# Kernel optimization log

Hardware: AMD Instinct MI355X
Metric: run time of the kernel (lower is better)

Reference implementation:

```python
import jax, jax.numpy as jnp
import numpy as np

B, T, C, H, N = 2, 1024, 1024, 16, 64
D_DECAY, D_AAA, D_MV, D_GATE = 64, 64, 32, 128
LN_EPS = 64e-5  # GroupNorm eps used by RWKV7 (1e-5 * head_size_divisor**2)


def setup_inputs():
    key = jax.random.key(0)
    ks = jax.random.split(key, 32)
    rn = lambda k, shape, s=1.0: jax.random.normal(k, shape, jnp.float32) * s
    p = {}
    p['x'] = rn(ks[0], (B, T, C))
    p['v_first'] = rn(ks[1], (B, T, C))
    for i, nm in enumerate(['x_r', 'x_w', 'x_k', 'x_v', 'x_a', 'x_g']):
        p[nm] = jax.random.uniform(ks[2 + i], (1, 1, C), jnp.float32)
    p['w1'] = rn(ks[8], (C, D_DECAY), 0.02); p['w2'] = rn(ks[9], (D_DECAY, C), 0.02); p['w0'] = rn(ks[10], (C,), 0.5)
    p['a1'] = rn(ks[11], (C, D_AAA), 0.02); p['a2'] = rn(ks[12], (D_AAA, C), 0.02); p['a0'] = rn(ks[13], (C,), 0.1)
    p['v1'] = rn(ks[14], (C, D_MV), 0.02); p['v2'] = rn(ks[15], (D_MV, C), 0.02); p['v0'] = rn(ks[16], (C,), 0.1)
    p['g1'] = rn(ks[17], (C, D_GATE), 0.02); p['g2'] = rn(ks[18], (D_GATE, C), 0.02)
    p['k_k'] = jax.random.uniform(ks[19], (1, 1, C), jnp.float32)
    p['k_a'] = jax.random.uniform(ks[20], (1, 1, C), jnp.float32)
    p['r_k'] = rn(ks[21], (H, N), 0.1)
    s = C ** -0.5
    p['W_r'] = rn(ks[22], (C, C), s); p['W_k'] = rn(ks[23], (C, C), s)
    p['W_v'] = rn(ks[24], (C, C), s); p['W_o'] = rn(ks[25], (C, C), s)
    p['ln_w'] = jnp.ones((C,), jnp.float32); p['ln_b'] = jnp.zeros((C,), jnp.float32)
    return p


def _rwkv7_op(r, w, k, v, a, b):
    # r,w,k,v,a,b: (B,T,C). Per-head matrix-state recurrence:
    #   S_t = S_{t-1} * diag(decay_t) + (S_{t-1} @ a_t) b_t^T + v_t k_t^T ; out_t = S_t @ r_t
    f = lambda z: z.reshape(B, T, H, N).astype(jnp.float32).transpose(1, 0, 2, 3)  # (T,B,H,N)
    r_, k_, v_, a_, b_ = f(r), f(k), f(v), f(a), f(b)
    d_ = jnp.exp(-jnp.exp(f(w)))  # decay in (0,1)

    def step(S, inp):
        rt, dt, kt, vt, at, bt = inp  # each (B,H,N)
        sa = jnp.einsum('bhij,bhj->bhi', S, at)
        S = S * dt[:, :, None, :] + sa[..., None] * bt[:, :, None, :] + vt[..., None] * kt[:, :, None, :]
        return S, jnp.einsum('bhij,bhj->bhi', S, rt)

    S0 = jnp.zeros((B, H, N, N), jnp.float32)
    _, out = jax.lax.scan(step, S0, (r_, d_, k_, v_, a_, b_))
    return out.transpose(1, 0, 2, 3).reshape(B, T, C)


def _forward(x, v_first, x_r, x_w, x_k, x_v, x_a, x_g, w1, w2, w0, a1, a2, a0,
             v1, v2, v0, g1, g2, k_k, k_a, r_k, W_r, W_k, W_v, W_o, ln_w, ln_b):
    xx = jnp.pad(x, ((0, 0), (1, 0), (0, 0)))[:, :T] - x  # token shift
    xr = x + xx * x_r; xw = x + xx * x_w; xk = x + xx * x_k
    xv = x + xx * x_v; xa = x + xx * x_a; xg = x + xx * x_g
    r = xr @ W_r
    w = -jax.nn.softplus(-(jnp.tanh(xw @ w1) @ w2 + w0)) - 0.5
    k = xk @ W_k
    v = xv @ W_v
    v = v + (v_first - v) * jax.nn.sigmoid(xv @ v1 @ v2 + v0)  # layer_id > 0 branch
    a = jax.nn.sigmoid(xa @ a1 @ a2 + a0)
    g = jax.nn.sigmoid(xg @ g1) @ g2
    kk = (k * k_k).reshape(B, T, H, N)
    kk = (kk / jnp.maximum(jnp.linalg.norm(kk, axis=-1, keepdims=True), 1e-12)).reshape(B, T, C)
    k = k * (1.0 + (a - 1.0) * k_a)
    y = _rwkv7_op(r, w, k, v, -kk, kk * a)
    # GroupNorm(H groups over C) applied per token
    yh = y.reshape(B, T, H, N)
    mu = yh.mean(-1, keepdims=True)
    var = yh.var(-1, keepdims=True)
    y = ((yh - mu) / jnp.sqrt(var + LN_EPS)).reshape(B, T, C) * ln_w + ln_b
    rh = r.reshape(B, T, H, N); kh = k.reshape(B, T, H, N); vh = v.reshape(B, T, H, N)
    y = y + ((rh * kh * r_k).sum(-1, keepdims=True) * vh).reshape(B, T, C)
    return (y * g) @ W_o


def reference(x, v_first, x_r, x_w, x_k, x_v, x_a, x_g, w1, w2, w0, a1, a2, a0,
              v1, v2, v0, g1, g2, k_k, k_a, r_k, W_r, W_k, W_v, W_o, ln_w, ln_b):
    out = _forward(x, v_first, x_r, x_w, x_k, x_v, x_a, x_g, w1, w2, w0, a1, a2, a0,
                   v1, v2, v0, g1, g2, k_k, k_a, r_k, W_r, W_k, W_v, W_o, ln_w, ln_b)
    return (out, v_first)
```

## Files before the change

### kernel.cpp

```cpp
#include <hip/hip_runtime.h>
#include <hip/hip_bf16.h>
#include <cstdint>
#include <cstddef>

typedef __hip_bfloat16 bf16;
typedef __bf16 bf16x8 __attribute__((ext_vector_type(8)));
typedef float f32x4 __attribute__((ext_vector_type(4)));

#define BB 2
#define TT 1024
#define CC 1024
#define HH 16
#define PKS 448

__device__ __forceinline__ bf16 f2b(float v){ return __float2bfloat16(v); }

__device__ __forceinline__ float oct_add(float x) {
    x += __int_as_float(__builtin_amdgcn_mov_dpp(__float_as_int(x), 0xB1, 0xF, 0xF, true));
    x += __int_as_float(__builtin_amdgcn_mov_dpp(__float_as_int(x), 0x4E, 0xF, 0xF, true));
    x += __int_as_float(__builtin_amdgcn_mov_dpp(__float_as_int(x), 0x141, 0xF, 0xF, true));
    return x;
}

struct TrDesc { const float* in; bf16* out; int R, S; };
struct TrArgs { TrDesc d[12]; };

__global__ __launch_bounds__(256) void transpose_batch(TrArgs args)
{
    TrDesc t = args.d[blockIdx.z];
    __shared__ float tile[32][33];
    int s0 = blockIdx.x * 32, r0 = blockIdx.y * 32;
    if (s0 >= t.S || r0 >= t.R) return;
    int tx = threadIdx.x & 31, ty = threadIdx.x >> 5;
#pragma unroll
    for (int i = 0; i < 4; i++) {
        int r = r0 + ty + i * 8, s = s0 + tx;
        if (r < t.R && s < t.S) tile[ty + i * 8][tx] = t.in[(size_t)r * t.S + s];
    }
    __syncthreads();
#pragma unroll
    for (int i = 0; i < 4; i++) {
        int s = s0 + ty + i * 8, r = r0 + tx;
        if (s < t.S && r < t.R) t.out[(size_t)s * t.R + r] = f2b(tile[tx][ty + i * 8]);
    }
}

__global__ __launch_bounds__(256) void mix_kernel(
    const float* __restrict__ x, const float* __restrict__ vfirst,
    const float* __restrict__ mr, const float* __restrict__ mw, const float* __restrict__ mk,
    const float* __restrict__ mv, const float* __restrict__ ma, const float* __restrict__ mg,
    bf16* __restrict__ xr, bf16* __restrict__ xw, bf16* __restrict__ xk,
    bf16* __restrict__ xv, bf16* __restrict__ xa, bf16* __restrict__ xg,
    float* __restrict__ vout)
{
    int row = blockIdx.x;
    int t = row & (TT - 1);
    size_t base = (size_t)row * CC;
    for (int c = threadIdx.x; c < CC; c += 256) {
        float xc = x[base + c];
        float xp = (t > 0) ? x[base - CC + c] : 0.f;
        float d = xp - xc;
        xr[base + c] = f2b(xc + d * mr[c]);
        xw[base + c] = f2b(xc + d * mw[c]);
        xk[base + c] = f2b(xc + d * mk[c]);
        xv[base + c] = f2b(xc + d * mv[c]);
        xa[base + c] = f2b(xc + d * ma[c]);
        xg[base + c] = f2b(xc + d * mg[c]);
        vout[base + c] = vfirst[base + c];
    }
}

template <class EmitF>
__device__ __forceinline__ void gemm_tile(const bf16* __restrict__ A, const bf16* __restrict__ BT,
                                          int K, int m0, int n0, EmitF emit)
{
    __shared__ __align__(16) bf16 Atile[128 * 32];
    __shared__ __align__(16) bf16 Btile[128 * 32];
    int tid = threadIdx.x;
    int w = tid >> 6, lane = tid & 63;
    int wr = w >> 1, wc = w & 1;
    int quad = lane >> 4, l16 = lane & 15;

    f32x4 zero = {0.f, 0.f, 0.f, 0.f};
    f32x4 acc[4][4];
#pragma unroll
    for (int i = 0; i < 4; i++)
#pragma unroll
        for (int j = 0; j < 4; j++) acc[i][j] = zero;

    int rr = lane >> 2;
    int cs = lane & 3;
    int ra0 = w * 32 + rr;
    int ra1 = ra0 + 16;
    int cg0 = cs ^ ((ra0 >> 1) & 3);
    int cg1 = cs ^ ((ra1 >> 1) & 3);

    for (int k0 = 0; k0 < K; k0 += 32) {
        uint4 av0 = *reinterpret_cast<const uint4*>(A  + (size_t)(m0 + ra0) * K + k0 + cg0 * 8);
        uint4 av1 = *reinterpret_cast<const uint4*>(A  + (size_t)(m0 + ra1) * K + k0 + cg1 * 8);
        uint4 bv0 = *reinterpret_cast<const uint4*>(BT + (size_t)(n0 + ra0) * K + k0 + cg0 * 8);
        uint4 bv1 = *reinterpret_cast<const uint4*>(BT + (size_t)(n0 + ra1) * K + k0 + cg1 * 8);
        __syncthreads();
        *reinterpret_cast<uint4*>(&Atile[ra0 * 32 + cs * 8]) = av0;
        *reinterpret_cast<uint4*>(&Atile[ra1 * 32 + cs * 8]) = av1;
        *reinterpret_cast<uint4*>(&Btile[ra0 * 32 + cs * 8]) = bv0;
        *reinterpret_cast<uint4*>(&Btile[ra1 * 32 + cs * 8]) = bv1;
        __syncthreads();

        bf16x8 af[4], bfr[4];
#pragma unroll
        for (int mi = 0; mi < 4; mi++) {
            int m = wr * 64 + mi * 16 + l16;
            int c2 = quad ^ ((m >> 1) & 3);
            af[mi] = *reinterpret_cast<const bf16x8*>(&Atile[m * 32 + c2 * 8]);
        }
#pragma unroll
        for (int ni = 0; ni < 4; ni++) {
            int n = wc * 64 + ni * 16 + l16;
            int c2 = quad ^ ((n >> 1) & 3);
            bfr[ni] = *reinterpret_cast<const bf16x8*>(&Btile[n * 32 + c2 * 8]);
        }
#pragma unroll
        for (int mi = 0; mi < 4; mi++)
#pragma unroll
            for (int ni = 0; ni < 4; ni++)
                acc[mi][ni] = __builtin_amdgcn_mfma_f32_16x16x32_bf16(af[mi], bfr[ni], acc[mi][ni], 0, 0, 0);
    }

#pragma unroll
    for (int mi = 0; mi < 4; mi++)
#pragma unroll
        for (int ni = 0; ni < 4; ni++)
#pragma unroll
            for (int rg = 0; rg < 4; rg++) {
                int m = m0 + wr * 64 + mi * 16 + quad * 4 + rg;
                int n = n0 + wc * 64 + ni * 16 + l16;
                emit(m, n, acc[mi][ni][rg]);
            }
}

struct B3Args { const bf16* A[3]; const bf16* BT[3]; float* out[3]; };
__global__ __launch_bounds__(256) void big3_kernel(B3Args args)
{
    int z = blockIdx.z;
    float* out = args.out[z];
    gemm_tile(args.A[z], args.BT[z], 1024, blockIdx.x * 128, blockIdx.y * 128,
              [&](int m, int n, float v) { out[(size_t)m * 1024 + n] = v; });
}

struct L1Desc { const bf16* A; const bf16* BT; bf16* outB; int N; int mode; };
struct L1Args { L1Desc d[4]; };
__global__ __launch_bounds__(256) void lora1_kernel(L1Args args)
{
    L1Desc dz = args.d[blockIdx.z];
    gemm_tile(dz.A, dz.BT, 1024, blockIdx.x * 128, 0,
              [&](int m, int n, float v) {
                  if (n < dz.N) {
                      float r = (dz.mode == 2) ? tanhf(v)
                              : (dz.mode == 3) ? 1.f / (1.f + expf(-v)) : v;
                      dz.outB[(size_t)m * dz.N + n] = f2b(r);
                  }
              });
}

struct L2Desc { const bf16* A; const bf16* BT; const float* bias; float* outF; int K; int mode; };
struct L2Args { L2Desc d[4]; const float* vraw; const float* vfirst; };
__global__ __launch_bounds__(256) void lora2_kernel(L2Args args)
{
    L2Desc dz = args.d[blockIdx.z];
    gemm_tile(dz.A, dz.BT, dz.K, blockIdx.x * 128, blockIdx.y * 128,
              [&](int m, int n, float v) {
                  size_t idx = (size_t)m * 1024 + n;
                  if (dz.mode == 4) {
                      float xx = v + dz.bias[n];
                      float ww = -log1pf(expf(-xx)) - 0.5f;
                      dz.outF[idx] = expf(-expf(ww));
                  } else if (dz.mode == 5) {
                      float xx = v + dz.bias[n];
                      dz.outF[idx] = 1.f / (1.f + expf(-xx));
                  } else if (dz.mode == 6) {
                      float gate = 1.f / (1.f + expf(-(v + dz.bias[n])));
                      float vr = args.vraw[idx];
                      dz.outF[idx] = vr + (args.vfirst[idx] - vr) * gate;
                  } else {
                      dz.outF[idx] = v;
                  }
              });
}

__global__ __launch_bounds__(256) void final_kernel(const bf16* __restrict__ A, const bf16* __restrict__ BT,
                                                    float* __restrict__ out)
{
    gemm_tile(A, BT, 1024, blockIdx.x * 128, blockIdx.y * 128,
              [&](int m, int n, float v) { out[(size_t)m * 1024 + n] = v; });
}

__global__ __launch_bounds__(256) void pack_kernel(
    float* __restrict__ k, const float* __restrict__ a, const float* __restrict__ r,
    const float* __restrict__ v, const float* __restrict__ dw,
    const float* __restrict__ kkw, const float* __restrict__ kaw,
    float* __restrict__ PK)
{
    int tid = threadIdx.x;
    int wave = tid >> 6, lane = tid & 63;
    int idx = blockIdx.x * 4 + wave;
    size_t off = (size_t)idx * 64 + lane;
    int c = (idx & 15) * 64 + lane;
    float kraw = k[off];
    float av = a[off];
    float kkv = kraw * kkw[c];
    float s = kkv * kkv;
#pragma unroll
    for (int m = 32; m; m >>= 1) s += __shfl_xor(s, m);
    float kkn = kkv / fmaxf(sqrtf(s), 1e-12f);
    float ks = kraw * (1.f + (av - 1.f) * kaw[c]);
    k[off] = ks;
    float bb = kkn * av;
    float rv = r[off];
    float dv = dw[off];
    float bt = bb * rv, ct = ks * rv;
#pragma unroll
    for (int m = 32; m; m >>= 1) { bt += __shfl_xor(bt, m); ct += __shfl_xor(ct, m); }
    int b = idx >> 14;
    int h = idx & 15;
    int t = (idx >> 4) & (TT - 1);
    size_t sidx = (size_t)(b * HH + h) * TT + t;
    float* pw = PK + sidx * PKS;
    pw[lane] = ks; pw[64 + lane] = kkn; pw[128 + lane] = bb; pw[192 + lane] = v[off];
    pw[256 + lane] = rv; pw[320 + lane] = dv;
    if (lane == 0) { pw[384] = bt; pw[385] = ct; }
}

struct StepS {
    f32x4 q[2], d[2], r[2], k[2], b[2];
    float vi; float2 bc;
};

__device__ __forceinline__ void load_stepS(StepS& s, const float* __restrict__ sb, int jc, int row)
{
#pragma unroll
    for (int m = 0; m < 2; m++) s.q[m] = *(const f32x4*)(sb + 64 + jc + 4 * m);
#pragma unroll
    for (int m = 0; m < 2; m++) s.d[m] = *(const f32x4*)(sb + 320 + jc + 4 * m);
#pragma unroll
    for (int m = 0; m < 2; m++) s.r[m] = *(const f32x4*)(sb + 256 + jc + 4 * m);
#pragma unroll
    for (int m = 0; m < 2; m++) s.k[m] = *(const f32x4*)(sb + jc + 4 * m);
#pragma unroll
    for (int m = 0; m < 2; m++) s.b[m] = *(const f32x4*)(sb + 128 + jc + 4 * m);
    s.vi = sb[192 + row];
    s.bc = *(const float2*)(sb + 384);
}

__device__ __forceinline__ float step_updateS(const StepS& sd, f32x4 S[2])
{
    f32x4 Sd0 = S[0] * sd.d[0];
    f32x4 Sd1 = S[1] * sd.d[1];
    f32x4 sac = S[0] * sd.q[0] + S[1] * sd.q[1];
    f32x4 oac = Sd0 * sd.r[0] + Sd1 * sd.r[1];
    float sar = (sac[0] + sac[1]) + (sac[2] + sac[3]);
    sar = oct_add(sar);
    float od = oct_add((oac[0] + oac[1]) + (oac[2] + oac[3]));
    float o = fmaf(sd.vi, sd.bc.y, fmaf(-sar, sd.bc.x, od));
    float sa = -sar;
    S[0] = Sd0 + sa * sd.b[0] + sd.vi * sd.k[0];
    S[1] = Sd1 + sa * sd.b[1] + sd.vi * sd.k[1];
    return o;
}

__global__ __launch_bounds__(64, 1) void scan_kernel(
    const float* __restrict__ PK, float* __restrict__ ybuf)
{
    const int lane = threadIdx.x;
    const int bh = blockIdx.x >> 3;
    const int b = bh >> 4, h = bh & 15;
    const int wq = blockIdx.x & 7;
    const int row = wq * 8 + (lane >> 3);
    const int jc = (lane & 7) * 8;

    f32x4 S[2];
    S[0] = (f32x4){0.f, 0.f, 0.f, 0.f};
    S[1] = (f32x4){0.f, 0.f, 0.f, 0.f};

    const float* sb = PK + (size_t)bh * TT * PKS;

    StepS A, B, C, D;
    load_stepS(A, sb,           jc, row);
    load_stepS(B, sb + PKS,     jc, row);
    load_stepS(C, sb + 2 * PKS, jc, row);
    load_stepS(D, sb + 3 * PKS, jc, row);
    sb += 4 * PKS;

    float* py = ybuf + (size_t)b * TT * CC + h * 64 + row;

    for (int t = 0; t < TT; t += 4) {
        float o = step_updateS(A, S);
        if ((lane & 7) == 0) *py = o;
        py += CC;
        load_stepS(A, sb, jc, row);
        __builtin_amdgcn_sched_barrier(0);

        o = step_updateS(B, S);
        if ((lane & 7) == 0) *py = o;
        py += CC;
        load_stepS(B, sb + PKS, jc, row);
        __builtin_amdgcn_sched_barrier(0);

        o = step_updateS(C, S);
        if ((lane & 7) == 0) *py = o;
        py += CC;
        load_stepS(C, sb + 2 * PKS, jc, row);
        __builtin_amdgcn_sched_barrier(0);

        o = step_updateS(D, S);
        if ((lane & 7) == 0) *py = o;
        py += CC;
        load_stepS(D, sb + 3 * PKS, jc, row);
        __builtin_amdgcn_sched_barrier(0);

        sb += 4 * PKS;
    }
}

__global__ __launch_bounds__(256) void gn_kernel(
    const float* __restrict__ y, const float* __restrict__ r, const float* __restrict__ k,
    const float* __restrict__ v, const float* __restrict__ g,
    const float* __restrict__ lnw, const float* __restrict__ lnb,
    const float* __restrict__ rk, bf16* __restrict__ z)
{
    int tid = threadIdx.x;
    int idx = blockIdx.x * 4 + (tid >> 6);
    int lane = tid & 63;
    size_t off = (size_t)idx * 64 + lane;
    int c = (idx & 15) * 64 + lane;
    float yv = y[off];
    float rv = r[off], kv = k[off], vv = v[off];
    float s1 = yv, s2 = yv * yv, s3 = rv * kv * rk[c];
#pragma unroll
    for (int m = 32; m; m >>= 1) {
        s1 += __shfl_xor(s1, m);
        s2 += __shfl_xor(s2, m);
        s3 += __shfl_xor(s3, m);
    }
    float mu = s1 * (1.f / 64.f);
    float var = fmaxf(s2 * (1.f / 64.f) - mu * mu, 0.f);
    float yn = (yv - mu) * rsqrtf(var + 64e-5f) * lnw[c] + lnb[c];
    float out = (yn + s3 * vv) * g[off];
    z[off] = f2b(out);
}

extern "C" void kernel_launch(void* const* d_in, const int* in_sizes, int n_in,
                              void* d_out, int out_size, void* d_ws, size_t ws_size,
                              hipStream_t stream)
{
    const float* x       = (const float*)d_in[0];
    const float* v_first = (const float*)d_in[1];
    const float* x_r = (const float*)d_in[2];
    const float* x_w = (const float*)d_in[3];
    const float* x_k = (const float*)d_in[4];
    const float* x_v = (const float*)d_in[5];
    const float* x_a = (const float*)d_in[6];
    const float* x_g = (const float*)d_in[7];
    const float* w1 = (const float*)d_in[8];
    const float* w2 = (const float*)d_in[9];
    const float* w0 = (const float*)d_in[10];
    const float* a1 = (const float*)d_in[11];
    const float* a2 = (const float*)d_in[12];
    const float* a0 = (const float*)d_in[13];
    const float* v1 = (const float*)d_in[14];
    const float* v2 = (const float*)d_in[15];
    const float* v0 = (const float*)d_in[16];
    const float* g1 = (const float*)d_in[17];
    const float* g2 = (const float*)d_in[18];
    const float* k_k = (const float*)d_in[19];
    const float* k_a = (const float*)d_in[20];
    const float* r_k = (const float*)d_in[21];
    const float* W_r = (const float*)d_in[22];
    const float* W_k = (const float*)d_in[23];
    const float* W_v = (const float*)d_in[24];
    const float* W_o = (const float*)d_in[25];
    const float* ln_w = (const float*)d_in[26];
    const float* ln_b = (const float*)d_in[27];

    const size_t BTC = (size_t)BB * TT * CC;
    const int M = BB * TT;

    char* ws = (char*)d_ws;
    size_t off = 0;
    auto alloc = [&](size_t bytes) -> char* {
        char* p = ws + off;
        off += (bytes + 255) & ~(size_t)255;
        return p;
    };

    bf16* xr = (bf16*)alloc(BTC * 2);
    bf16* xw = (bf16*)alloc(BTC * 2);
    bf16* xk = (bf16*)alloc(BTC * 2);
    bf16* xv = (bf16*)alloc(BTC * 2);
    bf16* xa = (bf16*)alloc(BTC * 2);
    bf16* xg = (bf16*)alloc(BTC * 2);
    bf16* WrT = (bf16*)alloc(1024 * 1024 * 2);
    bf16* WkT = (bf16*)alloc(1024 * 1024 * 2);
    bf16* WvT = (bf16*)alloc(1024 * 1024 * 2);
    bf16* w1T = (bf16*)alloc(128 * 1024 * 2);
    bf16* a1T = (bf16*)alloc(128 * 1024 * 2);
    bf16* v1T = (bf16*)alloc(128 * 1024 * 2);
    bf16* g1T = (bf16*)alloc(128 * 1024 * 2);
    bf16* w2T = (bf16*)alloc(1024 * 64 * 2);
    bf16* a2T = (bf16*)alloc(1024 * 64 * 2);
    bf16* v2T = (bf16*)alloc(1024 * 32 * 2);
    bf16* g2T = (bf16*)alloc(1024 * 128 * 2);
    bf16* h_w = (bf16*)alloc((size_t)M * 64 * 2);
    bf16* h_a = (bf16*)alloc((size_t)M * 64 * 2);
    bf16* h_v = (bf16*)alloc((size_t)M * 32 * 2);
    bf16* h_g = (bf16*)alloc((size_t)M * 128 * 2);

    float* PK = (float*)ws;
    size_t pk_end = (size_t)BB * HH * TT * PKS * 4;
    if (off < pk_end) off = pk_end;
    off = (off + 255) & ~(size_t)255;

    bf16* WoT = (bf16*)alloc(1024 * 1024 * 2);
    float* rbuf = (float*)alloc(BTC * 4);
    float* kbuf = (float*)alloc(BTC * 4);
    float* vraw = (float*)alloc(BTC * 4);
    float* vbuf = (float*)alloc(BTC * 4);
    float* dbuf = (float*)alloc(BTC * 4);
    float* abuf = (float*)alloc(BTC * 4);
    float* gbuf = (float*)alloc(BTC * 4);

    float* ybuf = vraw;
    bf16*  zbuf = (bf16*)dbuf;

    (void)in_sizes; (void)n_in; (void)out_size; (void)ws_size;

    TrArgs ta;
    ta.d[0]  = {W_r, WrT, 1024, 1024};
    ta.d[1]  = {W_k, WkT, 1024, 1024};
    ta.d[2]  = {W_v, WvT, 1024, 1024};
    ta.d[3]  = {W_o, WoT, 1024, 1024};
    ta.d[4]  = {w1, w1T, 1024, 64};
    ta.d[5]  = {a1, a1T, 1024, 64};
    ta.d[6]  = {v1, v1T, 1024, 32};
    ta.d[7]  = {g1, g1T, 1024, 128};
    ta.d[8]  = {w2, w2T, 64, 1024};
    ta.d[9]  = {a2, a2T, 64, 1024};
    ta.d[10] = {v2, v2T, 32, 1024};
    ta.d[11] = {g2, g2T, 128, 1024};
    transpose_batch<<<dim3(32, 32, 12), 256, 0, stream>>>(ta);

    float* vout = (float*)d_out + BTC;
    mix_kernel<<<BB * TT, 256, 0, stream>>>(x, v_first, x_r, x_w, x_k, x_v, x_a, x_g,
                                            xr, xw, xk, xv, xa, xg, vout);

    B3Args b3;
    b3.A[0] = xr; b3.A[1] = xk; b3.A[2] = xv;
    b3.BT[0] = WrT; b3.BT[1] = WkT; b3.BT[2] = WvT;
    b3.out[0] = rbuf; b3.out[1] = kbuf; b3.out[2] = vraw;
    big3_kernel<<<dim3(16, 8, 3), 256, 0, stream>>>(b3);

    L1Args l1;
    l1.d[0] = {xw, w1T, h_w, 64, 2};
    l1.d[1] = {xa, a1T, h_a, 64, 0};
    l1.d[2] = {xv, v1T, h_v, 32, 0};
    l1.d[3] = {xg, g1T, h_g, 128, 3};
    lora1_kernel<<<dim3(16, 1, 4), 256, 0, stream>>>(l1);

    L2Args l2;
    l2.d[0] = {h_w, w2T, w0, dbuf, 64, 4};
    l2.d[1] = {h_a, a2T, a0, abuf, 64, 5};
    l2.d[2] = {h_v, v2T, v0, vbuf, 32, 6};
    l2.d[3] = {h_g, g2T, nullptr, gbuf, 128, 0};
    l2.vraw = vraw; l2.vfirst = v_first;
    lora2_kernel<<<dim3(16, 8, 4), 256, 0, stream>>>(l2);

    pack_kernel<<<BB * TT * HH / 4, 256, 0, stream>>>(kbuf, abuf, rbuf, vbuf, dbuf, k_k, k_a, PK);

    scan_kernel<<<BB * HH * 8, 64, 0, stream>>>(PK, ybuf);

    gn_kernel<<<BB * TT * HH / 4, 256, 0, stream>>>(ybuf, rbuf, kbuf, vbuf, gbuf, ln_w, ln_b, r_k, zbuf);

    final_kernel<<<dim3(16, 8), 256, 0, stream>>>(zbuf, WoT, (float*)d_out);
}
```

Baseline: 490.8 us.

## Stream scan inputs through LDS ring with async global-to-LDS loads and split rows finer

The scan kernel now prefetches each timestep's packed inputs into an 8-slot LDS ring using global_load_lds, waiting on vmcnt and then reading the operands from LDS instead of holding four register sets loaded directly from global memory. Each wave now covers 4 state rows with 16 lanes per row holding 4 columns each, so the reduction gains an extra DPP stage and the grid doubles to 512 blocks. Block indices are remapped so that blocks sharing a (batch, head) land on the same XCD, which may improve L2 reuse. The intent is to hide global load latency on this serial recurrence and spread it across more CUs, at the cost of more blocks redundantly loading the same packed data and a longer reduction chain per step.

```diff
diff --git a/kernel.cpp b/kernel.cpp
--- a/kernel.cpp
+++ b/kernel.cpp
@@ -12,14 +12,24 @@
 #define CC 1024
 #define HH 16
 #define PKS 448
+#define PKB 1792
+#define RING 8
+#define SLOTB 2048
 
 __device__ __forceinline__ bf16 f2b(float v){ return __float2bfloat16(v); }
 
-__device__ __forceinline__ float oct_add(float x) {
+__device__ __forceinline__ float hex_add(float x) {
     x += __int_as_float(__builtin_amdgcn_mov_dpp(__float_as_int(x), 0xB1, 0xF, 0xF, true));
     x += __int_as_float(__builtin_amdgcn_mov_dpp(__float_as_int(x), 0x4E, 0xF, 0xF, true));
     x += __int_as_float(__builtin_amdgcn_mov_dpp(__float_as_int(x), 0x141, 0xF, 0xF, true));
+    x += __int_as_float(__builtin_amdgcn_mov_dpp(__float_as_int(x), 0x140, 0xF, 0xF, true));
     return x;
+}
+
+typedef __attribute__((address_space(3))) void as3_void;
+typedef __attribute__((address_space(1))) const void as1_void;
+__device__ __forceinline__ void gload_lds16(const void* g, void* l) {
+    __builtin_amdgcn_global_load_lds((as1_void*)g, (as3_void*)l, 16, 0, 0);
 }
 
 struct TrDesc { const float* in; bf16* out; int R, S; };
@@ -231,95 +241,94 @@
     if (lane == 0) { pw[384] = bt; pw[385] = ct; }
 }
 
-struct StepS {
-    f32x4 q[2], d[2], r[2], k[2], b[2];
-    float vi; float2 bc;
-};
-
-__device__ __forceinline__ void load_stepS(StepS& s, const float* __restrict__ sb, int jc, int row)
-{
-#pragma unroll
-    for (int m = 0; m < 2; m++) s.q[m] = *(const f32x4*)(sb + 64 + jc + 4 * m);
-#pragma unroll
-    for (int m = 0; m < 2; m++) s.d[m] = *(const f32x4*)(sb + 320 + jc + 4 * m);
-#pragma unroll
-    for (int m = 0; m < 2; m++) s.r[m] = *(const f32x4*)(sb + 256 + jc + 4 * m);
-#pragma unroll
-    for (int m = 0; m < 2; m++) s.k[m] = *(const f32x4*)(sb + jc + 4 * m);
-#pragma unroll
-    for (int m = 0; m < 2; m++) s.b[m] = *(const f32x4*)(sb + 128 + jc + 4 * m);
-    s.vi = sb[192 + row];
-    s.bc = *(const float2*)(sb + 384);
-}
-
-__device__ __forceinline__ float step_updateS(const StepS& sd, f32x4 S[2])
-{
-    f32x4 Sd0 = S[0] * sd.d[0];
-    f32x4 Sd1 = S[1] * sd.d[1];
-    f32x4 sac = S[0] * sd.q[0] + S[1] * sd.q[1];
-    f32x4 oac = Sd0 * sd.r[0] + Sd1 * sd.r[1];
-    float sar = (sac[0] + sac[1]) + (sac[2] + sac[3]);
-    sar = oct_add(sar);
-    float od = oct_add((oac[0] + oac[1]) + (oac[2] + oac[3]));
-    float o = fmaf(sd.vi, sd.bc.y, fmaf(-sar, sd.bc.x, od));
+struct SetR { f32x4 q, d, r, k, b; float vi; float2 bc; };
+
+__device__ __forceinline__ void ds_load_set(SetR& s, const char* slot, int c16, int row)
+{
+    s.q  = *(const f32x4*)(slot + 256  + c16);
+    s.d  = *(const f32x4*)(slot + 1280 + c16);
+    s.r  = *(const f32x4*)(slot + 1024 + c16);
+    s.k  = *(const f32x4*)(slot + 0    + c16);
+    s.b  = *(const f32x4*)(slot + 512  + c16);
+    s.vi = *(const float*)(slot + 768 + row * 4);
+    s.bc = *(const float2*)(slot + 1536);
+}
+
+__device__ __forceinline__ float step4(const SetR& sd, f32x4& S)
+{
+    f32x4 Sd   = S * sd.d;
+    f32x4 sacv = S * sd.q;
+    f32x4 oacv = Sd * sd.r;
+    float sar = (sacv[0] + sacv[1]) + (sacv[2] + sacv[3]);
+    float od  = (oacv[0] + oacv[1]) + (oacv[2] + oacv[3]);
+    sar = hex_add(sar);
+    od  = hex_add(od);
     float sa = -sar;
-    S[0] = Sd0 + sa * sd.b[0] + sd.vi * sd.k[0];
-    S[1] = Sd1 + sa * sd.b[1] + sd.vi * sd.k[1];
+    float o = fmaf(sd.vi, sd.bc.y, fmaf(sa, sd.bc.x, od));
+    S = Sd + sa * sd.b + sd.vi * sd.k;
     return o;
 }
 
 __global__ __launch_bounds__(64, 1) void scan_kernel(
     const float* __restrict__ PK, float* __restrict__ ybuf)
 {
+    __shared__ __align__(16) char ring[RING * SLOTB];
     const int lane = threadIdx.x;
-    const int bh = blockIdx.x >> 3;
+    const int xcd = blockIdx.x & 7, kk = blockIdx.x >> 3;
+    const int bh = xcd * 4 + (kk >> 4);
+    const int wq = kk & 15;
     const int b = bh >> 4, h = bh & 15;
-    const int wq = blockIdx.x & 7;
-    const int row = wq * 8 + (lane >> 3);
-    const int jc = (lane & 7) * 8;
-
-    f32x4 S[2];
-    S[0] = (f32x4){0.f, 0.f, 0.f, 0.f};
-    S[1] = (f32x4){0.f, 0.f, 0.f, 0.f};
-
-    const float* sb = PK + (size_t)bh * TT * PKS;
-
-    StepS A, B, C, D;
-    load_stepS(A, sb,           jc, row);
-    load_stepS(B, sb + PKS,     jc, row);
-    load_stepS(C, sb + 2 * PKS, jc, row);
-    load_stepS(D, sb + 3 * PKS, jc, row);
-    sb += 4 * PKS;
+    const int row = wq * 4 + (lane >> 4);
+    const int c = lane & 15;
+    const int c16 = c * 16;
+
+    f32x4 S = {0.f, 0.f, 0.f, 0.f};
+
+    const char* base = (const char*)(PK + (size_t)bh * TT * PKS);
+    const char* p1 = base + lane * 16;
+    const char* p2 = base + 1024 + lane * 16;
+
+#pragma unroll
+    for (int s = 0; s < RING; s++) {
+        gload_lds16(p1 + (size_t)s * PKB, ring + s * SLOTB);
+        gload_lds16(p2 + (size_t)s * PKB, ring + s * SLOTB + 1024);
+    }
+    p1 += (size_t)RING * PKB;
+    p2 += (size_t)RING * PKB;
+    asm volatile("s_waitcnt vmcnt(0)" ::: "memory");
+    __builtin_amdgcn_sched_barrier(0);
+
+    SetR A, B, C, D;
+    ds_load_set(A, ring + 0 * SLOTB, c16, row);
+    ds_load_set(B, ring + 1 * SLOTB, c16, row);
+    ds_load_set(C, ring + 2 * SLOTB, c16, row);
 
     float* py = ybuf + (size_t)b * TT * CC + h * 64 + row;
 
-    for (int t = 0; t < TT; t += 4) {
-        float o = step_updateS(A, S);
-        if ((lane & 7) == 0) *py = o;
-        py += CC;
-        load_stepS(A, sb, jc, row);
-        __builtin_amdgcn_sched_barrier(0);
-
-        o = step_updateS(B, S);
-        if ((lane & 7) == 0) *py = o;
-        py += CC;
-        load_stepS(B, sb + PKS, jc, row);
-        __builtin_amdgcn_sched_barrier(0);
-
-        o = step_updateS(C, S);
-        if ((lane & 7) == 0) *py = o;
-        py += CC;
-        load_stepS(C, sb + 2 * PKS, jc, row);
-        __builtin_amdgcn_sched_barrier(0);
-
-        o = step_updateS(D, S);
-        if ((lane & 7) == 0) *py = o;
-        py += CC;
-        load_stepS(D, sb + 3 * PKS, jc, row);
-        __builtin_amdgcn_sched_barrier(0);
-
-        sb += 4 * PKS;
-    }
+#define SCAN_BODY(SLOT, XV, PV)                                             \
+    {                                                                       \
+        float o = step4(XV, S);                                             \
+        if (c == 0) *py = o;                                                \
+        py += CC;                                                           \
+        gload_lds16(p1, ring + (SLOT) * SLOTB);                             \
+        gload_lds16(p2, ring + (SLOT) * SLOTB + 1024);                      \
+        p1 += PKB; p2 += PKB;                                               \
+        asm volatile("s_waitcnt vmcnt(15)" ::: "memory");                   \
+        __builtin_amdgcn_sched_barrier(0);                                  \
+        ds_load_set(PV, ring + (((SLOT) + 3) & 7) * SLOTB, c16, row);       \
+    }
+
+    for (int t = 0; t < TT; t += 8) {
+        SCAN_BODY(0, A, D)
+        SCAN_BODY(1, B, A)
+        SCAN_BODY(2, C, B)
+        SCAN_BODY(3, D, C)
+        SCAN_BODY(4, A, D)
+        SCAN_BODY(5, B, A)
+        SCAN_BODY(6, C, B)
+        SCAN_BODY(7, D, C)
+    }
+#undef SCAN_BODY
 }
 
 __global__ __launch_bounds__(256) void gn_kernel(
@@ -476,7 +485,7 @@
 
     pack_kernel<<<BB * TT * HH / 4, 256, 0, stream>>>(kbuf, abuf, rbuf, vbuf, dbuf, k_k, k_a, PK);
 
-    scan_kernel<<<BB * HH * 8, 64, 0, stream>>>(PK, ybuf);
+    scan_kernel<<<BB * HH * 16, 64, 0, stream>>>(PK, ybuf);
 
     gn_kernel<<<BB * TT * HH / 4, 256, 0, stream>>>(ybuf, rbuf, kbuf, vbuf, gbuf, ln_w, ln_b, r_k, zbuf);
 
```

Result: slower. 763.0 us (+55.5%).
